# Kernel tuning notes

Measured on AMD Instinct MI355X. Metric: run time of the kernel, lower is better.

## Reference

```python
import jax, jax.numpy as jnp
import numpy as np

INV_SQRT2 = np.float32(2.0 ** -0.5)
EPS = 1e-5


def _bn5(x, g, b, m, v):
    # inference-mode BatchNorm3d over channel axis 1 of NCDHW
    r = (1, -1, 1, 1, 1)
    return (x - m.reshape(r)) * (g.reshape(r) * jax.lax.rsqrt(v.reshape(r) + EPS)) + b.reshape(r)


def _conv3d(x, w, b, dil=1, pad=0):
    out = jax.lax.conv_general_dilated(
        x, w, window_strides=(1, 1, 1), padding=[(pad, pad)] * 3,
        rhs_dilation=(dil, dil, dil),
        dimension_numbers=('NCDHW', 'OIDHW', 'NCDHW'))
    return out + b.reshape(1, -1, 1, 1, 1)


def _haar_dwt2(x):
    # pywt dwt2(x, 'haar', axes=(-3,-2)) for even-length axes.
    # axis -3 (D): a = approx, d = detail (pywt sign: (x0 - x1)/sqrt2)
    a = (x[:, :, 0::2] + x[:, :, 1::2]) * INV_SQRT2
    d = (x[:, :, 0::2] - x[:, :, 1::2]) * INV_SQRT2
    # axis -2 (H)
    LL = (a[:, :, :, 0::2] + a[:, :, :, 1::2]) * INV_SQRT2  # 'aa'
    HL = (a[:, :, :, 0::2] - a[:, :, :, 1::2]) * INV_SQRT2  # 'ad'
    LH = (d[:, :, :, 0::2] + d[:, :, :, 1::2]) * INV_SQRT2  # 'da'
    HH = (d[:, :, :, 0::2] - d[:, :, :, 1::2]) * INV_SQRT2  # 'dd'
    return LL, LH, HL, HH


def setup_inputs() -> dict:
    key = jax.random.key(0)
    ks = jax.random.split(key, 12)
    B, C1, D, H, W = 2, 60, 128, 128, 64
    CH, R = 64, 4  # gate channels, CH // reduction_ratio
    f32 = jnp.float32
    inp = {
        'x1': jax.random.normal(ks[0], (B, C1, D // 2, H // 2, W), f32),
        'x2': jax.random.normal(ks[1], (B, 1, D, H, W), f32),
        # BatchNorm3d(4) on dwt features
        'bn_g': jnp.ones(4, f32), 'bn_b': jnp.zeros(4, f32),
        'bn_m': jnp.zeros(4, f32), 'bn_v': jnp.ones(4, f32),
        # BAM channel gate: Linear(64->4), BN1d(4), Linear(4->64)
        'cg_w1': jax.random.normal(ks[2], (R, CH), f32) * 0.05,
        'cg_b1': jnp.zeros(R, f32),
        'cg_bng': jnp.ones(R, f32), 'cg_bnb': jnp.zeros(R, f32),
        'cg_bnm': jnp.zeros(R, f32), 'cg_bnv': jnp.ones(R, f32),
        'cg_w2': jax.random.normal(ks[3], (CH, R), f32) * 0.05,
        'cg_b2': jnp.zeros(CH, f32),
        # BAM spatial gate
        'sg_w0': jax.random.normal(ks[4], (R, CH, 1, 1, 1), f32) * 0.05,
        'sg_b0': jnp.zeros(R, f32),
        'sg_g0': jnp.ones(R, f32), 'sg_be0': jnp.zeros(R, f32),
        'sg_m0': jnp.zeros(R, f32), 'sg_v0': jnp.ones(R, f32),
        'sg_w1': jax.random.normal(ks[5], (R, R, 3, 3, 3), f32) * 0.05,
        'sg_b1': jnp.zeros(R, f32),
        'sg_g1': jnp.ones(R, f32), 'sg_be1': jnp.zeros(R, f32),
        'sg_m1': jnp.zeros(R, f32), 'sg_v1': jnp.ones(R, f32),
        'sg_w2': jax.random.normal(ks[6], (R, R, 3, 3, 3), f32) * 0.05,
        'sg_b2': jnp.zeros(R, f32),
        'sg_g2': jnp.ones(R, f32), 'sg_be2': jnp.zeros(R, f32),
        'sg_m2': jnp.zeros(R, f32), 'sg_v2': jnp.ones(R, f32),
        'sg_w3': jax.random.normal(ks[7], (1, R, 1, 1, 1), f32) * 0.05,
        'sg_b3': jnp.zeros(1, f32),
    }
    return inp


def reference(x1, x2, bn_g, bn_b, bn_m, bn_v,
              cg_w1, cg_b1, cg_bng, cg_bnb, cg_bnm, cg_bnv, cg_w2, cg_b2,
              sg_w0, sg_b0, sg_g0, sg_be0, sg_m0, sg_v0,
              sg_w1, sg_b1, sg_g1, sg_be1, sg_m1, sg_v1,
              sg_w2, sg_b2, sg_g2, sg_be2, sg_m2, sg_v2,
              sg_w3, sg_b3):
    LL, LH, HL, HH = _haar_dwt2(x2)
    dwt = jnp.concatenate([LL, LH, HL, HH], axis=1)          # [B,4,D/2,H/2,W]
    dwt = jax.nn.relu(_bn5(dwt, bn_g, bn_b, bn_m, bn_v))
    feat = jnp.concatenate([dwt, x1], axis=1)                # [B,64,D/2,H/2,W]

    # BAM channel gate
    pooled = feat.mean(axis=(2, 3, 4))                        # [B,64]
    h = pooled @ cg_w1.T + cg_b1
    h = jax.nn.relu((h - cg_bnm) * (cg_bng * jax.lax.rsqrt(cg_bnv + EPS)) + cg_bnb)
    att_c = (h @ cg_w2.T + cg_b2)[:, :, None, None, None]     # [B,64,1,1,1]

    # BAM spatial gate
    s = jax.nn.relu(_bn5(_conv3d(feat, sg_w0, sg_b0), sg_g0, sg_be0, sg_m0, sg_v0))
    s = jax.nn.relu(_bn5(_conv3d(s, sg_w1, sg_b1, dil=4, pad=4), sg_g1, sg_be1, sg_m1, sg_v1))
    s = jax.nn.relu(_bn5(_conv3d(s, sg_w2, sg_b2, dil=4, pad=4), sg_g2, sg_be2, sg_m2, sg_v2))
    att_s = _conv3d(s, sg_w3, sg_b3)                          # [B,1,D/2,H/2,W]

    scale = 1.0 + jax.nn.sigmoid(att_c + att_s)
    return (feat * scale, LL)
```

## Files before the change

kernel.cpp:

```cpp
#include <hip/hip_runtime.h>
#include <math.h>

#define EPSBN 1e-5f

constexpr int B   = 2;
constexpr int C1  = 60;
constexpr int NV  = 64 * 64 * 64;
constexpr int NBa = NV / 512;

__global__ __launch_bounds__(256) void kA(
    const float* __restrict__ x1, const float* __restrict__ x2,
    const float* __restrict__ bn_g, const float* __restrict__ bn_b,
    const float* __restrict__ bn_m, const float* __restrict__ bn_v,
    const float* __restrict__ sg_w0, const float* __restrict__ sg_b0,
    const float* __restrict__ sg_g0, const float* __restrict__ sg_be0,
    const float* __restrict__ sg_m0, const float* __restrict__ sg_v0,
    float* __restrict__ dwtM, float* __restrict__ s0,
    float* __restrict__ part, float* __restrict__ outLL)
{
    __shared__ float w0l[256];
    __shared__ float cA[4], cB[4];
    __shared__ float dsc[4], dsh[4];
    __shared__ float wsum[64][4];

    const int tid = threadIdx.x;
    w0l[tid] = sg_w0[tid];
    if (tid < 4) {
        float sc = sg_g0[tid] * rsqrtf(sg_v0[tid] + EPSBN);
        cA[tid] = sc;
        cB[tid] = (sg_b0[tid] - sg_m0[tid]) * sc + sg_be0[tid];
        float d = bn_g[tid] * rsqrtf(bn_v[tid] + EPSBN);
        dsc[tid] = d;
        dsh[tid] = bn_b[tid] - bn_m[tid] * d;
    }
    __syncthreads();

    const int b = blockIdx.y;
    const int v = blockIdx.x * 512 + tid * 2;
    const int x = v & 63, y = (v >> 6) & 63, z = v >> 12;
    const int lane = tid & 63, wv = tid >> 6;

    const float* px2 = x2 + (size_t)b * (128 * 128 * 64);
    const size_t i00 = ((size_t)(2 * z) * 128 + 2 * y) * 64 + x;
    const float2 p00 = *(const float2*)(px2 + i00);
    const float2 p01 = *(const float2*)(px2 + i00 + 64);
    const float2 p10 = *(const float2*)(px2 + i00 + 8192);
    const float2 p11 = *(const float2*)(px2 + i00 + 8256);
    const float* q00 = (const float*)&p00; const float* q01 = (const float*)&p01;
    const float* q10 = (const float*)&p10; const float* q11 = (const float*)&p11;

    float tv[2][4], llv[2];
    #pragma unroll
    for (int vi = 0; vi < 2; ++vi) {
        float a = q00[vi], bb = q01[vi], c = q10[vi], d = q11[vi];
        float LL = 0.5f * (a + bb + c + d);
        float LH = 0.5f * (a + bb - c - d);
        float HL = 0.5f * (a - bb + c - d);
        float HH = 0.5f * (a - bb - c + d);
        llv[vi] = LL;
        tv[vi][0] = fmaxf(LL * dsc[0] + dsh[0], 0.f);
        tv[vi][1] = fmaxf(LH * dsc[1] + dsh[1], 0.f);
        tv[vi][2] = fmaxf(HL * dsc[2] + dsh[2], 0.f);
        tv[vi][3] = fmaxf(HH * dsc[3] + dsh[3], 0.f);
    }
    *(float2*)(outLL + (size_t)b * NV + v) = make_float2(llv[0], llv[1]);

    float acc[2][4] = {};
    #pragma unroll
    for (int c = 0; c < 4; ++c) {
        #pragma unroll
        for (int vi = 0; vi < 2; ++vi) {
            float t = tv[vi][c];
            #pragma unroll
            for (int r = 0; r < 4; ++r) acc[vi][r] += w0l[r * 64 + c] * t;
        }
        float rs = tv[0][c] + tv[1][c];
        #pragma unroll
        for (int off = 32; off; off >>= 1) rs += __shfl_xor(rs, off);
        if (lane == 0) wsum[c][wv] = rs;
        *(float2*)(dwtM + ((size_t)b * 4 + c) * NV + v) = make_float2(tv[0][c], tv[1][c]);
    }

    const float* px1 = x1 + (size_t)b * C1 * NV + v;
    for (int c = 0; c < C1; ++c) {
        const float2 f = *(const float2*)(px1 + (size_t)c * NV);
        #pragma unroll
        for (int r = 0; r < 4; ++r) {
            acc[0][r] += w0l[r * 64 + 4 + c] * f.x;
            acc[1][r] += w0l[r * 64 + 4 + c] * f.y;
        }
        float rs = f.x + f.y;
        #pragma unroll
        for (int off = 32; off; off >>= 1) rs += __shfl_xor(rs, off);
        if (lane == 0) wsum[4 + c][wv] = rs;
    }

    float4* ps0 = (float4*)s0 + (size_t)b * NV + v;
    #pragma unroll
    for (int vi = 0; vi < 2; ++vi)
        ps0[vi] = make_float4(fmaxf(acc[vi][0] * cA[0] + cB[0], 0.f),
                              fmaxf(acc[vi][1] * cA[1] + cB[1], 0.f),
                              fmaxf(acc[vi][2] * cA[2] + cB[2], 0.f),
                              fmaxf(acc[vi][3] * cA[3] + cB[3], 0.f));

    __syncthreads();
    if (tid < 64) {
        float p = wsum[tid][0] + wsum[tid][1] + wsum[tid][2] + wsum[tid][3];
        part[((size_t)b * 64 + tid) * NBa + blockIdx.x] = p;
    }
}

__global__ __launch_bounds__(256) void kConv1(
    const float* __restrict__ sin_,
    const float* __restrict__ w, const float* __restrict__ bias,
    const float* __restrict__ g, const float* __restrict__ be,
    const float* __restrict__ m, const float* __restrict__ vv,
    const float* __restrict__ part,
    const float* __restrict__ cg_w1, const float* __restrict__ cg_b1,
    const float* __restrict__ cg_bng, const float* __restrict__ cg_bnb,
    const float* __restrict__ cg_bnm, const float* __restrict__ cg_bnv,
    const float* __restrict__ cg_w2, const float* __restrict__ cg_b2,
    float* __restrict__ ec,
    float* __restrict__ outp)
{
    const int tid = threadIdx.x;
    const int b = blockIdx.y;

    if (blockIdx.x == NBa) {
        __shared__ float pooled[64];
        __shared__ float h[4];
        const int c = tid >> 2, q = tid & 3;
        const float4* pp = (const float4*)(part + ((size_t)b * 64 + c) * NBa + q * 128);
        float sm = 0.f;
        #pragma unroll
        for (int i = 0; i < 32; ++i) { float4 f = pp[i]; sm += f.x + f.y + f.z + f.w; }
        sm += __shfl_xor(sm, 1);
        sm += __shfl_xor(sm, 2);
        if (q == 0) pooled[c] = sm * (1.0f / NV);
        __syncthreads();
        if (tid < 4) {
            float a = cg_b1[tid];
            for (int cc = 0; cc < 64; ++cc) a += pooled[cc] * cg_w1[tid * 64 + cc];
            float sc = cg_bng[tid] * rsqrtf(cg_bnv[tid] + EPSBN);
            h[tid] = fmaxf((a - cg_bnm[tid]) * sc + cg_bnb[tid], 0.f);
        }
        __syncthreads();
        if (tid < 64) {
            float a = cg_b2[tid];
            #pragma unroll
            for (int r = 0; r < 4; ++r) a += h[r] * cg_w2[tid * 4 + r];
            ec[b * 64 + tid] = __expf(-a);
        }
        return;
    }

    __shared__ float wl[432];
    __shared__ float cA[4], cB[4];
    for (int i = tid; i < 432; i += 256) wl[i] = w[i];
    if (tid < 4) {
        float sc = g[tid] * rsqrtf(vv[tid] + EPSBN);
        cA[tid] = sc;
        cB[tid] = (bias[tid] - m[tid]) * sc + be[tid];
    }
    __syncthreads();

    const int v = blockIdx.x * 512 + tid * 2;
    const int x = v & 63, y = (v >> 6) & 63, z = v >> 12;
    const float4* pin = (const float4*)sin_ + (size_t)b * NV;

    float acc[2][4] = {};
    #pragma unroll
    for (int kz = -1; kz <= 1; ++kz) {
        const int zz = z + 4 * kz;
        if ((unsigned)zz >= 64u) continue;
        #pragma unroll
        for (int ky = -1; ky <= 1; ++ky) {
            const int yy = y + 4 * ky;
            if ((unsigned)yy >= 64u) continue;
            #pragma unroll
            for (int kx = -1; kx <= 1; ++kx) {
                const int xx = x + 4 * kx;
                if ((unsigned)xx >= 64u) continue;
                const int t = (kz + 1) * 9 + (ky + 1) * 3 + (kx + 1);
                const int vt = zz * 4096 + yy * 64 + xx;
                #pragma unroll
                for (int vi = 0; vi < 2; ++vi) {
                    const float4 tap = pin[vt + vi];
                    acc[vi][0] += wl[      t] * tap.x + wl[ 27 + t] * tap.y + wl[ 54 + t] * tap.z + wl[ 81 + t] * tap.w;
                    acc[vi][1] += wl[108 + t] * tap.x + wl[135 + t] * tap.y + wl[162 + t] * tap.z + wl[189 + t] * tap.w;
                    acc[vi][2] += wl[216 + t] * tap.x + wl[243 + t] * tap.y + wl[270 + t] * tap.z + wl[297 + t] * tap.w;
                    acc[vi][3] += wl[324 + t] * tap.x + wl[351 + t] * tap.y + wl[378 + t] * tap.z + wl[405 + t] * tap.w;
                }
            }
        }
    }

    float4* po = (float4*)outp + (size_t)b * NV + v;
    #pragma unroll
    for (int vi = 0; vi < 2; ++vi)
        po[vi] = make_float4(fmaxf(acc[vi][0] * cA[0] + cB[0], 0.f),
                             fmaxf(acc[vi][1] * cA[1] + cB[1], 0.f),
                             fmaxf(acc[vi][2] * cA[2] + cB[2], 0.f),
                             fmaxf(acc[vi][3] * cA[3] + cB[3], 0.f));
}

__global__ __launch_bounds__(256) void kConv2(
    const float* __restrict__ sin_,
    const float* __restrict__ w, const float* __restrict__ bias,
    const float* __restrict__ g, const float* __restrict__ be,
    const float* __restrict__ m, const float* __restrict__ vv,
    const float* __restrict__ w3, const float* __restrict__ b3,
    float* __restrict__ es)
{
    __shared__ float wl[432];
    __shared__ float cA[4], cB[4], w3l[4], b3l;
    const int tid = threadIdx.x;
    for (int i = tid; i < 432; i += 256) wl[i] = w[i];
    if (tid < 4) {
        float sc = g[tid] * rsqrtf(vv[tid] + EPSBN);
        cA[tid] = sc;
        cB[tid] = (bias[tid] - m[tid]) * sc + be[tid];
        w3l[tid] = w3[tid];
    }
    if (tid == 0) b3l = b3[0];
    __syncthreads();

    const int b = blockIdx.y;
    const int v = blockIdx.x * 512 + tid * 2;
    const int x = v & 63, y = (v >> 6) & 63, z = v >> 12;
    const float4* pin = (const float4*)sin_ + (size_t)b * NV;

    float acc[2][4] = {};
    #pragma unroll
    for (int kz = -1; kz <= 1; ++kz) {
        const int zz = z + 4 * kz;
        if ((unsigned)zz >= 64u) continue;
        #pragma unroll
        for (int ky = -1; ky <= 1; ++ky) {
            const int yy = y + 4 * ky;
            if ((unsigned)yy >= 64u) continue;
            #pragma unroll
            for (int kx = -1; kx <= 1; ++kx) {
                const int xx = x + 4 * kx;
                if ((unsigned)xx >= 64u) continue;
                const int t = (kz + 1) * 9 + (ky + 1) * 3 + (kx + 1);
                const int vt = zz * 4096 + yy * 64 + xx;
                #pragma unroll
                for (int vi = 0; vi < 2; ++vi) {
                    const float4 tap = pin[vt + vi];
                    acc[vi][0] += wl[      t] * tap.x + wl[ 27 + t] * tap.y + wl[ 54 + t] * tap.z + wl[ 81 + t] * tap.w;
                    acc[vi][1] += wl[108 + t] * tap.x + wl[135 + t] * tap.y + wl[162 + t] * tap.z + wl[189 + t] * tap.w;
                    acc[vi][2] += wl[216 + t] * tap.x + wl[243 + t] * tap.y + wl[270 + t] * tap.z + wl[297 + t] * tap.w;
                    acc[vi][3] += wl[324 + t] * tap.x + wl[351 + t] * tap.y + wl[378 + t] * tap.z + wl[405 + t] * tap.w;
                }
            }
        }
    }

    float ev[2];
    #pragma unroll
    for (int vi = 0; vi < 2; ++vi) {
        float r0 = fmaxf(acc[vi][0] * cA[0] + cB[0], 0.f);
        float r1 = fmaxf(acc[vi][1] * cA[1] + cB[1], 0.f);
        float r2 = fmaxf(acc[vi][2] * cA[2] + cB[2], 0.f);
        float r3 = fmaxf(acc[vi][3] * cA[3] + cB[3], 0.f);
        ev[vi] = __expf(-(b3l + w3l[0] * r0 + w3l[1] * r1 + w3l[2] * r2 + w3l[3] * r3));
    }
    *(float2*)(es + (size_t)b * NV + v) = make_float2(ev[0], ev[1]);
}

__global__ __launch_bounds__(256) void kMul(
    const float* __restrict__ x1,
    const float* __restrict__ dwtM,
    const float* __restrict__ es,
    const float* __restrict__ ec,
    float* __restrict__ out0)
{
    const int i0 = blockIdx.x * 256 + threadIdx.x;
    #pragma unroll 4
    for (int it = 0; it < 16; ++it) {
        const size_t idx = (size_t)i0 + (size_t)it * 524288;
        const int b  = (int)(idx >> 22);
        const int r  = (int)(idx & 4194303);
        const int c  = r >> 16;
        const int vq = r & 65535;
        const float* base = (c < 4)
            ? dwtM + ((size_t)b * 4 + c) * NV
            : x1   + ((size_t)b * C1 + (c - 4)) * NV;
        const float4 in4 = *(const float4*)(base + (size_t)vq * 4);
        const float4 es4 = ((const float4*)(es + (size_t)b * NV))[vq];
        const float  e   = ec[(b << 6) + c];
        float4 o;
        o.x = in4.x * (1.f + __builtin_amdgcn_rcpf(1.f + e * es4.x));
        o.y = in4.y * (1.f + __builtin_amdgcn_rcpf(1.f + e * es4.y));
        o.z = in4.z * (1.f + __builtin_amdgcn_rcpf(1.f + e * es4.z));
        o.w = in4.w * (1.f + __builtin_amdgcn_rcpf(1.f + e * es4.w));
        ((float4*)out0)[idx] = o;
    }
}

extern "C" void kernel_launch(void* const* d_in, const int* in_sizes, int n_in,
                              void* d_out, int out_size, void* d_ws, size_t ws_size,
                              hipStream_t stream)
{
    const float* x1 = (const float*)d_in[0];
    const float* x2 = (const float*)d_in[1];
    const float* bn_g = (const float*)d_in[2];
    const float* bn_b = (const float*)d_in[3];
    const float* bn_m = (const float*)d_in[4];
    const float* bn_v = (const float*)d_in[5];
    const float* cg_w1 = (const float*)d_in[6];
    const float* cg_b1 = (const float*)d_in[7];
    const float* cg_bng = (const float*)d_in[8];
    const float* cg_bnb = (const float*)d_in[9];
    const float* cg_bnm = (const float*)d_in[10];
    const float* cg_bnv = (const float*)d_in[11];
    const float* cg_w2 = (const float*)d_in[12];
    const float* cg_b2 = (const float*)d_in[13];
    const float* sg_w0 = (const float*)d_in[14];
    const float* sg_b0 = (const float*)d_in[15];
    const float* sg_g0 = (const float*)d_in[16];
    const float* sg_be0 = (const float*)d_in[17];
    const float* sg_m0 = (const float*)d_in[18];
    const float* sg_v0 = (const float*)d_in[19];
    const float* sg_w1 = (const float*)d_in[20];
    const float* sg_b1 = (const float*)d_in[21];
    const float* sg_g1 = (const float*)d_in[22];
    const float* sg_be1 = (const float*)d_in[23];
    const float* sg_m1 = (const float*)d_in[24];
    const float* sg_v1 = (const float*)d_in[25];
    const float* sg_w2 = (const float*)d_in[26];
    const float* sg_b2 = (const float*)d_in[27];
    const float* sg_g2 = (const float*)d_in[28];
    const float* sg_be2 = (const float*)d_in[29];
    const float* sg_m2 = (const float*)d_in[30];
    const float* sg_v2 = (const float*)d_in[31];
    const float* sg_w3 = (const float*)d_in[32];
    const float* sg_b3 = (const float*)d_in[33];

    float* ws = (float*)d_ws;
    float* dwtM = ws;
    float* s0   = ws + 2097152;
    float* s1   = ws + 4194304;
    float* es   = ws + 6291456;
    float* part = ws + 6815744;
    float* ec   = ws + 6881280;

    float* out0  = (float*)d_out;
    float* outLL = out0 + (size_t)B * 64 * NV;

    dim3 blk(256);
    kA<<<dim3(NBa, B), blk, 0, stream>>>(x1, x2, bn_g, bn_b, bn_m, bn_v,
                                         sg_w0, sg_b0, sg_g0, sg_be0, sg_m0, sg_v0,
                                         dwtM, s0, part, outLL);
    kConv1<<<dim3(NBa + 1, B), blk, 0, stream>>>(s0, sg_w1, sg_b1, sg_g1, sg_be1, sg_m1, sg_v1,
                                                 part, cg_w1, cg_b1, cg_bng, cg_bnb, cg_bnm, cg_bnv,
                                                 cg_w2, cg_b2, ec, s1);
    kConv2<<<dim3(NBa, B), blk, 0, stream>>>(s1, sg_w2, sg_b2, sg_g2, sg_be2, sg_m2, sg_v2,
                                             sg_w3, sg_b3, es);
    kMul<<<dim3(2048), blk, 0, stream>>>(x1, dwtM, es, ec, out0);
}
```

Before: 118.0 us.

## Use nontemporal output stores, scalar weights, float4 conv weights, and shallower shuffle reductions

Several independent micro-optimizations land at once. The large final output and the LL output now use nontemporal stores to reduce cache pollution. kA reads its weights and BN constants straight from global memory as uniform scalars instead of staging them in LDS. Its channel-sum reduction shuffles only across quads, which adds LDS writes and a 64-wide serial sum per channel. The dilated convs pack their weights into float4 LDS entries so each tap needs four vector LDS reads instead of sixteen scalar ones.

New measurement: 108.2 us. 8.3% less time.

```diff
diff --git a/kernel.cpp b/kernel.cpp
--- a/kernel.cpp
+++ b/kernel.cpp
@@ -2,6 +2,9 @@
 #include <math.h>
 
 #define EPSBN 1e-5f
+
+typedef float f32x2 __attribute__((ext_vector_type(2)));
+typedef float f32x4 __attribute__((ext_vector_type(4)));
 
 constexpr int B   = 2;
 constexpr int C1  = 60;
@@ -18,27 +21,23 @@
     float* __restrict__ dwtM, float* __restrict__ s0,
     float* __restrict__ part, float* __restrict__ outLL)
 {
-    __shared__ float w0l[256];
-    __shared__ float cA[4], cB[4];
-    __shared__ float dsc[4], dsh[4];
-    __shared__ float wsum[64][4];
+    __shared__ float wsumq[64][65];
 
     const int tid = threadIdx.x;
-    w0l[tid] = sg_w0[tid];
-    if (tid < 4) {
-        float sc = sg_g0[tid] * rsqrtf(sg_v0[tid] + EPSBN);
-        cA[tid] = sc;
-        cB[tid] = (sg_b0[tid] - sg_m0[tid]) * sc + sg_be0[tid];
-        float d = bn_g[tid] * rsqrtf(bn_v[tid] + EPSBN);
-        dsc[tid] = d;
-        dsh[tid] = bn_b[tid] - bn_m[tid] * d;
-    }
-    __syncthreads();
+    const int qid = tid >> 2;
+
+    float dsc[4], dsh[4], c0A[4], c0B[4];
+    #pragma unroll
+    for (int r = 0; r < 4; ++r) {
+        float d = bn_g[r] * rsqrtf(bn_v[r] + EPSBN);
+        dsc[r] = d; dsh[r] = bn_b[r] - bn_m[r] * d;
+        float sc = sg_g0[r] * rsqrtf(sg_v0[r] + EPSBN);
+        c0A[r] = sc; c0B[r] = (sg_b0[r] - sg_m0[r]) * sc + sg_be0[r];
+    }
 
     const int b = blockIdx.y;
     const int v = blockIdx.x * 512 + tid * 2;
     const int x = v & 63, y = (v >> 6) & 63, z = v >> 12;
-    const int lane = tid & 63, wv = tid >> 6;
 
     const float* px2 = x2 + (size_t)b * (128 * 128 * 64);
     const size_t i00 = ((size_t)(2 * z) * 128 + 2 * y) * 64 + x;
@@ -63,7 +62,10 @@
         tv[vi][2] = fmaxf(HL * dsc[2] + dsh[2], 0.f);
         tv[vi][3] = fmaxf(HH * dsc[3] + dsh[3], 0.f);
     }
-    *(float2*)(outLL + (size_t)b * NV + v) = make_float2(llv[0], llv[1]);
+    {
+        f32x2 ll2 = { llv[0], llv[1] };
+        __builtin_nontemporal_store(ll2, (f32x2*)(outLL + (size_t)b * NV + v));
+    }
 
     float acc[2][4] = {};
     #pragma unroll
@@ -72,40 +74,45 @@
         for (int vi = 0; vi < 2; ++vi) {
             float t = tv[vi][c];
             #pragma unroll
-            for (int r = 0; r < 4; ++r) acc[vi][r] += w0l[r * 64 + c] * t;
+            for (int r = 0; r < 4; ++r) acc[vi][r] += sg_w0[r * 64 + c] * t;
         }
         float rs = tv[0][c] + tv[1][c];
-        #pragma unroll
-        for (int off = 32; off; off >>= 1) rs += __shfl_xor(rs, off);
-        if (lane == 0) wsum[c][wv] = rs;
+        rs += __shfl_xor(rs, 1);
+        rs += __shfl_xor(rs, 2);
+        if ((tid & 3) == 0) wsumq[c][qid] = rs;
         *(float2*)(dwtM + ((size_t)b * 4 + c) * NV + v) = make_float2(tv[0][c], tv[1][c]);
     }
 
     const float* px1 = x1 + (size_t)b * C1 * NV + v;
+    #pragma unroll 2
     for (int c = 0; c < C1; ++c) {
         const float2 f = *(const float2*)(px1 + (size_t)c * NV);
         #pragma unroll
         for (int r = 0; r < 4; ++r) {
-            acc[0][r] += w0l[r * 64 + 4 + c] * f.x;
-            acc[1][r] += w0l[r * 64 + 4 + c] * f.y;
+            const float w = sg_w0[r * 64 + 4 + c];
+            acc[0][r] += w * f.x;
+            acc[1][r] += w * f.y;
         }
         float rs = f.x + f.y;
-        #pragma unroll
-        for (int off = 32; off; off >>= 1) rs += __shfl_xor(rs, off);
-        if (lane == 0) wsum[4 + c][wv] = rs;
+        rs += __shfl_xor(rs, 1);
+        rs += __shfl_xor(rs, 2);
+        if ((tid & 3) == 0) wsumq[4 + c][qid] = rs;
     }
 
     float4* ps0 = (float4*)s0 + (size_t)b * NV + v;
     #pragma unroll
     for (int vi = 0; vi < 2; ++vi)
-        ps0[vi] = make_float4(fmaxf(acc[vi][0] * cA[0] + cB[0], 0.f),
-                              fmaxf(acc[vi][1] * cA[1] + cB[1], 0.f),
-                              fmaxf(acc[vi][2] * cA[2] + cB[2], 0.f),
-                              fmaxf(acc[vi][3] * cA[3] + cB[3], 0.f));
+        ps0[vi] = make_float4(fmaxf(acc[vi][0] * c0A[0] + c0B[0], 0.f),
+                              fmaxf(acc[vi][1] * c0A[1] + c0B[1], 0.f),
+                              fmaxf(acc[vi][2] * c0A[2] + c0B[2], 0.f),
+                              fmaxf(acc[vi][3] * c0A[3] + c0B[3], 0.f));
 
     __syncthreads();
     if (tid < 64) {
-        float p = wsum[tid][0] + wsum[tid][1] + wsum[tid][2] + wsum[tid][3];
+        const float* rowp = &wsumq[tid][0];
+        float p = 0.f;
+        #pragma unroll
+        for (int i = 0; i < 64; ++i) p += rowp[i];
         part[((size_t)b * 64 + tid) * NBa + blockIdx.x] = p;
     }
 }
@@ -154,13 +161,18 @@
         return;
     }
 
-    __shared__ float wl[432];
-    __shared__ float cA[4], cB[4];
-    for (int i = tid; i < 432; i += 256) wl[i] = w[i];
-    if (tid < 4) {
-        float sc = g[tid] * rsqrtf(vv[tid] + EPSBN);
-        cA[tid] = sc;
-        cB[tid] = (bias[tid] - m[tid]) * sc + be[tid];
+    __shared__ float4 wl4[108];
+    if (tid < 108) {
+        const int t = tid >> 2, r = tid & 3;
+        wl4[tid] = make_float4(w[r * 108 +      t], w[r * 108 +  27 + t],
+                               w[r * 108 + 54 + t], w[r * 108 +  81 + t]);
+    }
+    float cAr[4], cBr[4];
+    #pragma unroll
+    for (int r = 0; r < 4; ++r) {
+        float sc = g[r] * rsqrtf(vv[r] + EPSBN);
+        cAr[r] = sc;
+        cBr[r] = (bias[r] - m[r]) * sc + be[r];
     }
     __syncthreads();
 
@@ -183,13 +195,17 @@
                 if ((unsigned)xx >= 64u) continue;
                 const int t = (kz + 1) * 9 + (ky + 1) * 3 + (kx + 1);
                 const int vt = zz * 4096 + yy * 64 + xx;
+                const float4 w0 = wl4[t * 4 + 0];
+                const float4 w1 = wl4[t * 4 + 1];
+                const float4 w2 = wl4[t * 4 + 2];
+                const float4 w3 = wl4[t * 4 + 3];
                 #pragma unroll
                 for (int vi = 0; vi < 2; ++vi) {
                     const float4 tap = pin[vt + vi];
-                    acc[vi][0] += wl[      t] * tap.x + wl[ 27 + t] * tap.y + wl[ 54 + t] * tap.z + wl[ 81 + t] * tap.w;
-                    acc[vi][1] += wl[108 + t] * tap.x + wl[135 + t] * tap.y + wl[162 + t] * tap.z + wl[189 + t] * tap.w;
-                    acc[vi][2] += wl[216 + t] * tap.x + wl[243 + t] * tap.y + wl[270 + t] * tap.z + wl[297 + t] * tap.w;
-                    acc[vi][3] += wl[324 + t] * tap.x + wl[351 + t] * tap.y + wl[378 + t] * tap.z + wl[405 + t] * tap.w;
+                    acc[vi][0] += w0.x * tap.x + w0.y * tap.y + w0.z * tap.z + w0.w * tap.w;
+                    acc[vi][1] += w1.x * tap.x + w1.y * tap.y + w1.z * tap.z + w1.w * tap.w;
+                    acc[vi][2] += w2.x * tap.x + w2.y * tap.y + w2.z * tap.z + w2.w * tap.w;
+                    acc[vi][3] += w3.x * tap.x + w3.y * tap.y + w3.z * tap.z + w3.w * tap.w;
                 }
             }
         }
@@ -198,10 +214,10 @@
     float4* po = (float4*)outp + (size_t)b * NV + v;
     #pragma unroll
     for (int vi = 0; vi < 2; ++vi)
-        po[vi] = make_float4(fmaxf(acc[vi][0] * cA[0] + cB[0], 0.f),
-                             fmaxf(acc[vi][1] * cA[1] + cB[1], 0.f),
-                             fmaxf(acc[vi][2] * cA[2] + cB[2], 0.f),
-                             fmaxf(acc[vi][3] * cA[3] + cB[3], 0.f));
+        po[vi] = make_float4(fmaxf(acc[vi][0] * cAr[0] + cBr[0], 0.f),
+                             fmaxf(acc[vi][1] * cAr[1] + cBr[1], 0.f),
+                             fmaxf(acc[vi][2] * cAr[2] + cBr[2], 0.f),
+                             fmaxf(acc[vi][3] * cAr[3] + cBr[3], 0.f));
 }
 
 __global__ __launch_bounds__(256) void kConv2(
@@ -212,17 +228,22 @@
     const float* __restrict__ w3, const float* __restrict__ b3,
     float* __restrict__ es)
 {
-    __shared__ float wl[432];
-    __shared__ float cA[4], cB[4], w3l[4], b3l;
     const int tid = threadIdx.x;
-    for (int i = tid; i < 432; i += 256) wl[i] = w[i];
-    if (tid < 4) {
-        float sc = g[tid] * rsqrtf(vv[tid] + EPSBN);
-        cA[tid] = sc;
-        cB[tid] = (bias[tid] - m[tid]) * sc + be[tid];
-        w3l[tid] = w3[tid];
-    }
-    if (tid == 0) b3l = b3[0];
+    __shared__ float4 wl4[108];
+    if (tid < 108) {
+        const int t = tid >> 2, r = tid & 3;
+        wl4[tid] = make_float4(w[r * 108 +      t], w[r * 108 +  27 + t],
+                               w[r * 108 + 54 + t], w[r * 108 +  81 + t]);
+    }
+    float cAr[4], cBr[4], w3l[4];
+    #pragma unroll
+    for (int r = 0; r < 4; ++r) {
+        float sc = g[r] * rsqrtf(vv[r] + EPSBN);
+        cAr[r] = sc;
+        cBr[r] = (bias[r] - m[r]) * sc + be[r];
+        w3l[r] = w3[r];
+    }
+    const float b3l = b3[0];
     __syncthreads();
 
     const int b = blockIdx.y;
@@ -245,13 +266,17 @@
                 if ((unsigned)xx >= 64u) continue;
                 const int t = (kz + 1) * 9 + (ky + 1) * 3 + (kx + 1);
                 const int vt = zz * 4096 + yy * 64 + xx;
+                const float4 w0 = wl4[t * 4 + 0];
+                const float4 w1 = wl4[t * 4 + 1];
+                const float4 w2 = wl4[t * 4 + 2];
+                const float4 w3q = wl4[t * 4 + 3];
                 #pragma unroll
                 for (int vi = 0; vi < 2; ++vi) {
                     const float4 tap = pin[vt + vi];
-                    acc[vi][0] += wl[      t] * tap.x + wl[ 27 + t] * tap.y + wl[ 54 + t] * tap.z + wl[ 81 + t] * tap.w;
-                    acc[vi][1] += wl[108 + t] * tap.x + wl[135 + t] * tap.y + wl[162 + t] * tap.z + wl[189 + t] * tap.w;
-                    acc[vi][2] += wl[216 + t] * tap.x + wl[243 + t] * tap.y + wl[270 + t] * tap.z + wl[297 + t] * tap.w;
-                    acc[vi][3] += wl[324 + t] * tap.x + wl[351 + t] * tap.y + wl[378 + t] * tap.z + wl[405 + t] * tap.w;
+                    acc[vi][0] += w0.x * tap.x + w0.y * tap.y + w0.z * tap.z + w0.w * tap.w;
+                    acc[vi][1] += w1.x * tap.x + w1.y * tap.y + w1.z * tap.z + w1.w * tap.w;
+                    acc[vi][2] += w2.x * tap.x + w2.y * tap.y + w2.z * tap.z + w2.w * tap.w;
+                    acc[vi][3] += w3q.x * tap.x + w3q.y * tap.y + w3q.z * tap.z + w3q.w * tap.w;
                 }
             }
         }
@@ -260,10 +285,10 @@
     float ev[2];
     #pragma unroll
     for (int vi = 0; vi < 2; ++vi) {
-        float r0 = fmaxf(acc[vi][0] * cA[0] + cB[0], 0.f);
-        float r1 = fmaxf(acc[vi][1] * cA[1] + cB[1], 0.f);
-        float r2 = fmaxf(acc[vi][2] * cA[2] + cB[2], 0.f);
-        float r3 = fmaxf(acc[vi][3] * cA[3] + cB[3], 0.f);
+        float r0 = fmaxf(acc[vi][0] * cAr[0] + cBr[0], 0.f);
+        float r1 = fmaxf(acc[vi][1] * cAr[1] + cBr[1], 0.f);
+        float r2 = fmaxf(acc[vi][2] * cAr[2] + cBr[2], 0.f);
+        float r3 = fmaxf(acc[vi][3] * cAr[3] + cBr[3], 0.f);
         ev[vi] = __expf(-(b3l + w3l[0] * r0 + w3l[1] * r1 + w3l[2] * r2 + w3l[3] * r3));
     }
     *(float2*)(es + (size_t)b * NV + v) = make_float2(ev[0], ev[1]);
@@ -290,12 +315,12 @@
         const float4 in4 = *(const float4*)(base + (size_t)vq * 4);
         const float4 es4 = ((const float4*)(es + (size_t)b * NV))[vq];
         const float  e   = ec[(b << 6) + c];
-        float4 o;
+        f32x4 o;
         o.x = in4.x * (1.f + __builtin_amdgcn_rcpf(1.f + e * es4.x));
         o.y = in4.y * (1.f + __builtin_amdgcn_rcpf(1.f + e * es4.y));
         o.z = in4.z * (1.f + __builtin_amdgcn_rcpf(1.f + e * es4.z));
         o.w = in4.w * (1.f + __builtin_amdgcn_rcpf(1.f + e * es4.w));
-        ((float4*)out0)[idx] = o;
+        __builtin_nontemporal_store(o, (f32x4*)out0 + idx);
     }
 }
 
```
